# Optimization experiments

Measured on AMD Instinct MI355X. Metric: run time of the kernel, lower is better.

## Reference

```python
import jax, jax.numpy as jnp
import numpy as np

N = 50000      # total atoms in batched graph
E = 800000     # edges
IN = 128       # in_feats
OUT = 64       # out_feats (per GAT head)
H = 4          # num_heads
NEG_SLOPE = 0.2
BN_EPS = 1e-5


def setup_inputs() -> dict:
    key = jax.random.key(0)
    ks = jax.random.split(key, 16)
    s = 0.1  # keep activations well-scaled
    return {
        "node_feats": jax.random.normal(ks[0], (N, IN), jnp.float32),
        "W_fc":       jax.random.normal(ks[1], (IN, H * OUT), jnp.float32) * s,
        "attn_l":     jax.random.normal(ks[2], (H, OUT), jnp.float32) * s,
        "attn_r":     jax.random.normal(ks[3], (H, OUT), jnp.float32) * s,
        "gat_res_w":  jax.random.normal(ks[4], (IN, H * OUT), jnp.float32) * s,
        "gat_bias":   jax.random.normal(ks[5], (H * OUT,), jnp.float32) * s,
        "conv_w":     jax.random.normal(ks[6], (1, H, 1), jnp.float32) * s,
        "conv_b":     jax.random.normal(ks[7], (1,), jnp.float32) * s,
        "res_w":      jax.random.normal(ks[8], (IN, OUT), jnp.float32) * s,
        "res_b":      jax.random.normal(ks[9], (OUT,), jnp.float32) * s,
        "bn_gamma":   jnp.ones((OUT,), jnp.float32),
        "bn_beta":    jnp.zeros((OUT,), jnp.float32),
        "src":        jax.random.randint(ks[10], (E,), 0, N, jnp.int32),
        "dst":        jax.random.randint(ks[11], (E,), 0, N, jnp.int32),
        "etype":      0,
    }


def reference(node_feats, W_fc, attn_l, attn_r, gat_res_w, gat_bias,
              conv_w, conv_b, res_w, res_b, bn_gamma, bn_beta,
              src, dst, etype):
    # ---- GATConv (DGL semantics, eval mode: no dropout) ----
    h = (node_feats @ W_fc).reshape(-1, H, OUT)            # [N,H,D]
    el = jnp.sum(h * attn_l, axis=-1)                      # [N,H]
    er = jnp.sum(h * attn_r, axis=-1)                      # [N,H]
    e = jax.nn.leaky_relu(el[src] + er[dst], NEG_SLOPE)    # [E,H]
    # segment softmax over incoming edges of each dst node
    m = jax.ops.segment_max(e, dst, num_segments=N)        # [N,H]
    m = jnp.where(jnp.isfinite(m), m, 0.0)                 # empty segments
    a = jnp.exp(e - m[dst])                                # [E,H]
    ssum = jax.ops.segment_sum(a, dst, num_segments=N)     # [N,H]
    alpha = a / (ssum[dst] + 1e-16)                        # [E,H]
    # weighted aggregation: rst[v] = sum_{(u->v)} alpha * h[u]
    rst = jax.ops.segment_sum(alpha[:, :, None] * h[src], dst, num_segments=N)  # [N,H,D]
    # GAT residual (in != H*OUT -> linear res_fc, no bias) + bias + activation
    rst = rst + (node_feats @ gat_res_w).reshape(-1, H, OUT) + gat_bias.reshape(H, OUT)
    rst = jax.nn.relu(rst)                                 # [N,H,D]
    # ---- Conv1d(4 -> 1, kernel=1): weighted head merge ----
    y = jnp.einsum("nhd,h->nd", rst, conv_w[0, :, 0]) + conv_b[0]  # [N,D]
    # ---- outer residual ----
    y = y + jax.nn.relu(node_feats @ res_w + res_b)
    # ---- BatchNorm1d (training-style batch stats) ----
    mean = jnp.mean(y, axis=0)
    var = jnp.var(y, axis=0)
    return (y - mean) / jnp.sqrt(var + BN_EPS) * bn_gamma + bn_beta
```

## Files before the change

### kernel.cpp

```cpp
#include <hip/hip_runtime.h>

#define IN_F   128
#define OUTD   64
#define HOUT   256
#define NEG_SLOPE 0.2f
#define BN_EPS 1e-5f
#define HB     1024
#define SB     512

typedef __attribute__((ext_vector_type(8))) short bf16x8;
typedef __attribute__((ext_vector_type(4))) float f32x4;
typedef __attribute__((ext_vector_type(2))) float f32x2;

__device__ __forceinline__ unsigned short f2bf(float f) {
    union { float f; unsigned u; } v; v.f = f;
    unsigned r = (v.u + 0x7FFF + ((v.u >> 16) & 1)) >> 16;
    return (unsigned short)r;
}
__device__ __forceinline__ float bf2f(unsigned short h) {
    union { unsigned u; float f; } v; v.u = ((unsigned)h) << 16;
    return v.f;
}
__device__ __forceinline__ float u2f(unsigned u) {
    union { unsigned u; float f; } v; v.u = u;
    return v.f;
}
__device__ __forceinline__ unsigned f2u(float f) {
    union { float f; unsigned u; } v; v.f = f;
    return v.u;
}

__device__ __forceinline__ int b2idx(int c, int k) {
    int tt, j;
    if (c < 256)      { tt = (c >> 4) & 3;                     j = c >> 6; }
    else if (c < 512) { int cc = c - 256; tt = 4 + ((cc >> 4) & 3); j = cc >> 6; }
    else if (c < 576) { int cc = c - 512; tt = 8;              j = cc >> 4; }
    else              { tt = 9;                                j = 0; }
    int n15 = c & 15;
    int ks = k >> 5, qd = (k >> 3) & 3, kk = k & 7;
    return ((((tt * 4 + j) * 4 + ks) * 64) + qd * 16 + n15) * 8 + kk;
}

__global__ __launch_bounds__(256) void k0_pack(
    const float* __restrict__ W_fc, const float* __restrict__ W_gres,
    const float* __restrict__ W_res,
    const float* __restrict__ attn_l, const float* __restrict__ attn_r,
    unsigned short* __restrict__ Btg2,
    const int* __restrict__ dst, int* __restrict__ degree,
    int* __restrict__ rank, int E)
{
    int bid = blockIdx.x, t = threadIdx.x;
    if (bid < 288) {
        int idx = bid * 256 + t;
        int c = idx >> 7, k = idx & 127;
        float v;
        if (c < 256)      v = W_fc[k * HOUT + c];
        else if (c < 512) v = W_gres[k * HOUT + (c - 256)];
        else              v = W_res[k * OUTD + (c - 512)];
        Btg2[b2idx(c, k)] = f2bf(v);
        return;
    }
    if (bid == 288) {
        for (int p = t; p < 512; p += 256) {
            int h = p >> 7, k = p & 127;
            float sl = 0.f, sr = 0.f;
            for (int d = 0; d < 64; ++d) {
                float wv = W_fc[k * HOUT + h * 64 + d];
                sl += wv * attn_l[h * 64 + d];
                sr += wv * attn_r[h * 64 + d];
            }
            Btg2[b2idx(576 + h, k)] = f2bf(sl);
            Btg2[b2idx(580 + h, k)] = f2bf(sr);
        }
        for (int p = t; p < 8 * 128; p += 256) {
            int c = 584 + (p >> 7), k = p & 127;
            Btg2[b2idx(c, k)] = 0;
        }
        return;
    }
    int ht = (bid - 289) * 256 + t;
    for (int e = ht; e < E; e += HB * 256)
        rank[e] = atomicAdd(degree + dst[e], 1);
}

__global__ __launch_bounds__(256) void k1_gemm(
    const float* __restrict__ A, const unsigned short* __restrict__ Btg2,
    const float* __restrict__ gat_bias, const float* __restrict__ res_b,
    const int* __restrict__ src, const int* __restrict__ dst,
    const int* __restrict__ rank, const int* __restrict__ excl,
    const int* __restrict__ blocksum, int* __restrict__ base,
    unsigned* __restrict__ usrc_sorted,
    unsigned char* __restrict__ Hh8, unsigned char* __restrict__ Hr8,
    unsigned short* __restrict__ Rres,
    float* __restrict__ el, float* __restrict__ er,
    int N, int E, int Gblocks, int nb)
{
    int t = threadIdx.x;

    if (blockIdx.x >= Gblocks) {
        __shared__ int sm[256];
        __shared__ int base_lds[256];
        int sb = blockIdx.x - Gblocks;
        int d0 = (t < nb) ? blocksum[t] : 0;
        sm[t] = d0; __syncthreads();
        for (int off = 1; off < 256; off <<= 1) {
            int v = (t >= off) ? sm[t - off] : 0;
            __syncthreads();
            sm[t] += v;
            __syncthreads();
        }
        base_lds[t] = sm[t] - d0;
        if (sb == 0) base[t] = sm[t] - d0;
        __syncthreads();
        for (int e = sb * 256 + t; e < E; e += SB * 256) {
            int d = dst[e];
            int p = excl[d] + base_lds[d >> 8] + rank[e];
            usrc_sorted[p] = (unsigned)src[e] << 8;
        }
        return;
    }

    int w = t >> 6, lane = t & 63, quad = lane >> 4, n15 = lane & 15;
    int gw = blockIdx.x * 4 + w;
    int T = (N + 15) / 16;
    if (gw >= T) return;

    int m0 = gw * 16;
    bool full = (m0 + 16 <= N);
    int lofs = (quad * 16 + n15) * 8;

    bf16x8 af[4];
    {
        int r = m0 + n15;
#pragma unroll
        for (int ks = 0; ks < 4; ++ks) {
            float4 v0 = make_float4(0.f, 0.f, 0.f, 0.f), v1 = v0;
            if (r < N) {
                const float* ap = A + (size_t)r * IN_F + ks * 32 + quad * 8;
                v0 = *(const float4*)ap;
                v1 = *(const float4*)(ap + 4);
            }
            bf16x8 o;
            o[0] = f2bf(v0.x); o[1] = f2bf(v0.y); o[2] = f2bf(v0.z); o[3] = f2bf(v0.w);
            o[4] = f2bf(v1.x); o[5] = f2bf(v1.y); o[6] = f2bf(v1.z); o[7] = f2bf(v1.w);
            af[ks] = o;
        }
    }

#pragma unroll
    for (int s = 0; s < 4; ++s) {
        bf16x8 bfr[4][4];
#pragma unroll
        for (int ks = 0; ks < 4; ++ks)
#pragma unroll
            for (int j = 0; j < 4; ++j)
                bfr[ks][j] = *(const bf16x8*)(Btg2 + ((s * 16 + j * 4 + ks) << 9) + lofs);
        f32x4 acc[4] = {};
#pragma unroll
        for (int ks = 0; ks < 4; ++ks)
#pragma unroll
            for (int j = 0; j < 4; ++j)
                acc[j] = __builtin_amdgcn_mfma_f32_16x16x32_bf16(af[ks], bfr[ks][j], acc[j], 0, 0, 0);
#pragma unroll
        for (int reg = 0; reg < 4; ++reg) {
            int r = m0 + quad * 4 + reg;
            if (full || r < N) {
                unsigned pk = (unsigned)__builtin_amdgcn_cvt_pk_fp8_f32(acc[0][reg], acc[1][reg], 0, false);
                pk = (unsigned)__builtin_amdgcn_cvt_pk_fp8_f32(acc[2][reg], acc[3][reg], (int)pk, true);
                *(unsigned*)(Hh8 + ((size_t)r << 8) + (s * 16 + n15) * 4) = pk;
            }
        }
    }

#pragma unroll
    for (int s = 0; s < 4; ++s) {
        bf16x8 bfr[4][4];
#pragma unroll
        for (int ks = 0; ks < 4; ++ks)
#pragma unroll
            for (int j = 0; j < 4; ++j)
                bfr[ks][j] = *(const bf16x8*)(Btg2 + (((4 + s) * 16 + j * 4 + ks) << 9) + lofs);
        f32x4 acc[4] = {};
#pragma unroll
        for (int ks = 0; ks < 4; ++ks)
#pragma unroll
            for (int j = 0; j < 4; ++j)
                acc[j] = __builtin_amdgcn_mfma_f32_16x16x32_bf16(af[ks], bfr[ks][j], acc[j], 0, 0, 0);
        float b0 = gat_bias[0 * 64 + s * 16 + n15];
        float b1 = gat_bias[1 * 64 + s * 16 + n15];
        float b2 = gat_bias[2 * 64 + s * 16 + n15];
        float b3 = gat_bias[3 * 64 + s * 16 + n15];
#pragma unroll
        for (int reg = 0; reg < 4; ++reg) {
            int r = m0 + quad * 4 + reg;
            if (full || r < N) {
                unsigned pk = (unsigned)__builtin_amdgcn_cvt_pk_fp8_f32(acc[0][reg] + b0, acc[1][reg] + b1, 0, false);
                pk = (unsigned)__builtin_amdgcn_cvt_pk_fp8_f32(acc[2][reg] + b2, acc[3][reg] + b3, (int)pk, true);
                *(unsigned*)(Hr8 + ((size_t)r << 8) + (s * 16 + n15) * 4) = pk;
            }
        }
    }

    {
        bf16x8 bfr[4][4];
#pragma unroll
        for (int ks = 0; ks < 4; ++ks)
#pragma unroll
            for (int j = 0; j < 4; ++j)
                bfr[ks][j] = *(const bf16x8*)(Btg2 + ((8 * 16 + j * 4 + ks) << 9) + lofs);
        f32x4 acc[4] = {};
#pragma unroll
        for (int ks = 0; ks < 4; ++ks)
#pragma unroll
            for (int j = 0; j < 4; ++j)
                acc[j] = __builtin_amdgcn_mfma_f32_16x16x32_bf16(af[ks], bfr[ks][j], acc[j], 0, 0, 0);
#pragma unroll
        for (int reg = 0; reg < 4; ++reg) {
            int r = m0 + quad * 4 + reg;
            if (full || r < N) {
#pragma unroll
                for (int j = 0; j < 4; ++j)
                    Rres[(size_t)r * OUTD + j * 16 + n15] = f2bf(acc[j][reg] + res_b[j * 16 + n15]);
            }
        }
    }

    {
        bf16x8 b4[4];
#pragma unroll
        for (int ks = 0; ks < 4; ++ks)
            b4[ks] = *(const bf16x8*)(Btg2 + ((9 * 16 + ks) << 9) + lofs);
        f32x4 acc2 = {};
#pragma unroll
        for (int ks = 0; ks < 4; ++ks)
            acc2 = __builtin_amdgcn_mfma_f32_16x16x32_bf16(af[ks], b4[ks], acc2, 0, 0, 0);
#pragma unroll
        for (int reg = 0; reg < 4; ++reg) {
            int r = m0 + quad * 4 + reg;
            if ((full || r < N) && n15 < 8) {
                float v = acc2[reg];
                if (n15 < 4) el[(size_t)r * 4 + n15] = v;
                else         er[(size_t)r * 4 + (n15 - 4)] = v;
            }
        }
    }
}

__global__ __launch_bounds__(256) void scanA_kernel(const int* __restrict__ degree,
                                                    int* __restrict__ excl,
                                                    int* __restrict__ blocksum, int N) {
    __shared__ int sm[256];
    int t = threadIdx.x;
    int i = blockIdx.x * 256 + t;
    int d = (i < N) ? degree[i] : 0;
    sm[t] = d; __syncthreads();
    for (int off = 1; off < 256; off <<= 1) {
        int v = (t >= off) ? sm[t - off] : 0;
        __syncthreads();
        sm[t] += v;
        __syncthreads();
    }
    if (i < N) excl[i] = sm[t] - d;
    if (t == 255) blocksum[blockIdx.x] = sm[255];
}

__global__ __launch_bounds__(256) void agg_kernel(
    const unsigned char* __restrict__ Hh8, const unsigned char* __restrict__ Hr8,
    const unsigned short* __restrict__ Rres, const float* __restrict__ el,
    const float* __restrict__ er,
    const int* __restrict__ excl, const int* __restrict__ base,
    const unsigned* __restrict__ usrc_sorted,
    const float* __restrict__ conv_w, const float* __restrict__ conv_b,
    float* __restrict__ y, float* __restrict__ bnsum8, float* __restrict__ bnsq8,
    int N, int E)
{
    __shared__ float smem[256];
    __shared__ float smem2[256];
    int t = threadIdx.x;
    int wave = t >> 6, lane = t & 63;
    int v = blockIdx.x * 4 + wave;

    float yv = 0.f;
    if (v < N) {
        int b  = excl[v] + base[v >> 8];
        int e2 = (v + 1 < N) ? (excl[v + 1] + base[(v + 1) >> 8]) : E;
        int deg = e2 - b;

        float4 rv = *(const float4*)(er + (size_t)v * 4);
        const unsigned char* hbase = Hh8 + lane * 4;
        float a0 = 0.f, a1 = 0.f, a2 = 0.f, a3 = 0.f;
        float p0 = 0.f, p1 = 0.f, p2 = 0.f, p3 = 0.f;

        for (int i0 = 0; i0 < deg; i0 += 64) {
            int j = i0 + lane;
            unsigned ux = 0;
            float s0 = 0.f, s1 = 0.f, s2 = 0.f, s3 = 0.f;
            if (j < deg) {
                ux = usrc_sorted[b + j];
                float4 l = *(const float4*)(el + ((size_t)(ux >> 8)) * 4);
                float x;
                x = l.x + rv.x; x = x > 0.f ? x : NEG_SLOPE * x; s0 = __expf(x);
                x = l.y + rv.y; x = x > 0.f ? x : NEG_SLOPE * x; s1 = __expf(x);
                x = l.z + rv.z; x = x > 0.f ? x : NEG_SLOPE * x; s2 = __expf(x);
                x = l.w + rv.w; x = x > 0.f ? x : NEG_SLOPE * x; s3 = __expf(x);
                p0 += s0; p1 += s1; p2 += s2; p3 += s3;
            }
            int cl = deg - i0; if (cl > 64) cl = 64;
            int jj = 0;
            for (; jj + 3 < cl; jj += 4) {
                unsigned u_[4], hv[4];
                float w0[4], w1[4], w2[4], w3[4];
#pragma unroll
                for (int k = 0; k < 4; ++k) {
                    u_[k] = (unsigned)__builtin_amdgcn_readlane((int)ux, jj + k);
                    w0[k] = u2f((unsigned)__builtin_amdgcn_readlane((int)f2u(s0), jj + k));
                    w1[k] = u2f((unsigned)__builtin_amdgcn_readlane((int)f2u(s1), jj + k));
                    w2[k] = u2f((unsigned)__builtin_amdgcn_readlane((int)f2u(s2), jj + k));
                    w3[k] = u2f((unsigned)__builtin_amdgcn_readlane((int)f2u(s3), jj + k));
                }
#pragma unroll
                for (int k = 0; k < 4; ++k)
                    hv[k] = *(const unsigned*)(hbase + u_[k]);
#pragma unroll
                for (int k = 0; k < 4; ++k) {
                    f32x2 lo = __builtin_amdgcn_cvt_pk_f32_fp8(hv[k], false);
                    f32x2 hi = __builtin_amdgcn_cvt_pk_f32_fp8(hv[k], true);
                    a0 += w0[k] * lo.x;
                    a1 += w1[k] * lo.y;
                    a2 += w2[k] * hi.x;
                    a3 += w3[k] * hi.y;
                }
            }
            for (; jj < cl; ++jj) {
                unsigned uA = (unsigned)__builtin_amdgcn_readlane((int)ux, jj);
                float w0 = u2f((unsigned)__builtin_amdgcn_readlane((int)f2u(s0), jj));
                float w1 = u2f((unsigned)__builtin_amdgcn_readlane((int)f2u(s1), jj));
                float w2 = u2f((unsigned)__builtin_amdgcn_readlane((int)f2u(s2), jj));
                float w3 = u2f((unsigned)__builtin_amdgcn_readlane((int)f2u(s3), jj));
                unsigned hvA = *(const unsigned*)(hbase + uA);
                f32x2 lo = __builtin_amdgcn_cvt_pk_f32_fp8(hvA, false);
                f32x2 hi = __builtin_amdgcn_cvt_pk_f32_fp8(hvA, true);
                a0 += w0 * lo.x;
                a1 += w1 * lo.y;
                a2 += w2 * hi.x;
                a3 += w3 * hi.y;
            }
        }
#pragma unroll
        for (int off = 1; off < 64; off <<= 1) {
            p0 += __shfl_xor(p0, off); p1 += __shfl_xor(p1, off);
            p2 += __shfl_xor(p2, off); p3 += __shfl_xor(p3, off);
        }
        float r0 = 1.f / (p0 + 1e-16f), r1 = 1.f / (p1 + 1e-16f);
        float r2 = 1.f / (p2 + 1e-16f), r3 = 1.f / (p3 + 1e-16f);

        unsigned hr = *(const unsigned*)(Hr8 + ((size_t)v << 8) + lane * 4);
        f32x2 rlo = __builtin_amdgcn_cvt_pk_f32_fp8(hr, false);
        f32x2 rhi = __builtin_amdgcn_cvt_pk_f32_fp8(hr, true);
        float resv = bf2f(Rres[(size_t)v * OUTD + lane]);
        yv = conv_b[0] + (resv > 0.f ? resv : 0.f);
        float tt;
        tt = a0 * r0 + rlo.x; tt = tt > 0.f ? tt : 0.f; yv += conv_w[0] * tt;
        tt = a1 * r1 + rlo.y; tt = tt > 0.f ? tt : 0.f; yv += conv_w[1] * tt;
        tt = a2 * r2 + rhi.x; tt = tt > 0.f ? tt : 0.f; yv += conv_w[2] * tt;
        tt = a3 * r3 + rhi.y; tt = tt > 0.f ? tt : 0.f; yv += conv_w[3] * tt;
        y[(size_t)v * OUTD + lane] = yv;
    }

    smem[t] = yv;
    smem2[t] = yv * yv;
    __syncthreads();
    if (t < 64) {
        float s = smem[t] + smem[t + 64] + smem[t + 128] + smem[t + 192];
        float q = smem2[t] + smem2[t + 64] + smem2[t + 128] + smem2[t + 192];
        int c = (blockIdx.x & 7) << 6;
        atomicAdd(bnsum8 + c + t, s);
        atomicAdd(bnsq8 + c + t, q);
    }
}

__global__ __launch_bounds__(256) void norm_kernel(
    const float* __restrict__ y,
    const float* __restrict__ bnsum8, const float* __restrict__ bnsq8,
    const float* __restrict__ gamma, const float* __restrict__ beta,
    float* __restrict__ out, int total4, float invN) {
    __shared__ float scale[64], shift[64];
    int t = threadIdx.x;
    if (t < 64) {
        float s = 0.f, q = 0.f;
#pragma unroll
        for (int c = 0; c < 8; ++c) { s += bnsum8[c * 64 + t]; q += bnsq8[c * 64 + t]; }
        float mean = s * invN;
        float var = q * invN - mean * mean;
        float sc = gamma[t] * rsqrtf(var + BN_EPS);
        scale[t] = sc;
        shift[t] = beta[t] - mean * sc;
    }
    __syncthreads();
    int idx = blockIdx.x * blockDim.x + t;
    if (idx >= total4) return;
    float4 v = *(const float4*)(y + (size_t)idx * 4);
    int d = (idx * 4) & 63;
    float4 o;
    o.x = v.x * scale[d + 0] + shift[d + 0];
    o.y = v.y * scale[d + 1] + shift[d + 1];
    o.z = v.z * scale[d + 2] + shift[d + 2];
    o.w = v.w * scale[d + 3] + shift[d + 3];
    *(float4*)(out + (size_t)idx * 4) = o;
}

extern "C" void kernel_launch(void* const* d_in, const int* in_sizes, int n_in,
                              void* d_out, int out_size, void* d_ws, size_t ws_size,
                              hipStream_t stream) {
    const float* node_feats = (const float*)d_in[0];
    const float* W_fc       = (const float*)d_in[1];
    const float* attn_l     = (const float*)d_in[2];
    const float* attn_r     = (const float*)d_in[3];
    const float* gat_res_w  = (const float*)d_in[4];
    const float* gat_bias   = (const float*)d_in[5];
    const float* conv_w     = (const float*)d_in[6];
    const float* conv_b     = (const float*)d_in[7];
    const float* res_w      = (const float*)d_in[8];
    const float* res_b      = (const float*)d_in[9];
    const float* bn_gamma   = (const float*)d_in[10];
    const float* bn_beta    = (const float*)d_in[11];
    const int*   src        = (const int*)d_in[12];
    const int*   dst        = (const int*)d_in[13];

    const int N = in_sizes[0] / IN_F;
    const int E = in_sizes[12];
    const int nb = (N + 255) / 256;
    const int T = (N + 15) / 16;
    const int Gblocks = (T + 3) / 4;

    char* ws = (char*)d_ws;
    size_t off = 0;
    auto alloc = [&](size_t bytes) -> void* {
        void* p = (void*)(ws + off);
        off += (bytes + 255) & ~(size_t)255;
        return p;
    };

    int*   degree  = (int*)alloc((size_t)N * 4);
    float* bnsum8  = (float*)alloc(8 * 64 * 4);
    float* bnsq8   = (float*)alloc(8 * 64 * 4);
    size_t zero_bytes = off;
    int*            rank        = (int*)alloc((size_t)E * 4);
    int*            excl        = (int*)alloc((size_t)N * 4);
    int*            blocksum    = (int*)alloc(256 * 4);
    int*            base        = (int*)alloc(256 * 4);
    unsigned*       usrc_sorted = (unsigned*)alloc((size_t)E * 4);
    unsigned short* Btg2        = (unsigned short*)alloc((size_t)10 * 16 * 512 * 2);
    unsigned char*  Hh8         = (unsigned char*)alloc((size_t)N * 256);
    unsigned char*  Hr8         = (unsigned char*)alloc((size_t)N * 256);
    unsigned short* Rres        = (unsigned short*)alloc((size_t)N * OUTD * 2);
    float*          el          = (float*)alloc((size_t)N * 4 * 4);
    float*          er          = (float*)alloc((size_t)N * 4 * 4);
    float*          y           = (float*)alloc((size_t)N * OUTD * 4);
    (void)ws_size; (void)n_in; (void)out_size;

    hipMemsetAsync(d_ws, 0, zero_bytes, stream);

    k0_pack<<<289 + HB, 256, 0, stream>>>(W_fc, gat_res_w, res_w, attn_l, attn_r, Btg2,
                                          dst, degree, rank, E);
    scanA_kernel<<<nb, 256, 0, stream>>>(degree, excl, blocksum, N);
    k1_gemm<<<Gblocks + SB, 256, 0, stream>>>(node_feats, Btg2, gat_bias, res_b,
                                              src, dst, rank, excl, blocksum, base,
                                              usrc_sorted, Hh8, Hr8, Rres,
                                              el, er, N, E, Gblocks, nb);
    agg_kernel<<<(N + 3) / 4, 256, 0, stream>>>(Hh8, Hr8, Rres, el, er, excl, base,
                                                usrc_sorted, conv_w, conv_b, y,
                                                bnsum8, bnsq8, N, E);
    norm_kernel<<<(N * OUTD / 4 + 255) / 256, 256, 0, stream>>>(y, bnsum8, bnsq8,
                                                                bn_gamma, bn_beta, (float*)d_out,
                                                                N * OUTD / 4, 1.f / (float)N);
}
```

Before: 226.9 us.

## Process four destination nodes per wave in GAT aggregation kernel

Each wave now handles four consecutive destination nodes instead of one, walking their combined edge range in 64-edge chunks. The low two bits of each sorted source entry carry the local node index, and four accumulator vectors are selected per edge. Per-node softmax denominators are gathered with LDS atomics rather than wave shuffles. This targets underused lanes and per-chunk overhead for low-degree nodes (average degree is about 16), at the cost of a per-edge switch, LDS atomic contention and a scattered er load per edge.

```diff
diff --git a/kernel.cpp b/kernel.cpp
--- a/kernel.cpp
+++ b/kernel.cpp
@@ -115,7 +115,7 @@
         for (int e = sb * 256 + t; e < E; e += SB * 256) {
             int d = dst[e];
             int p = excl[d] + base_lds[d >> 8] + rank[e];
-            usrc_sorted[p] = (unsigned)src[e] << 8;
+            usrc_sorted[p] = ((unsigned)src[e] << 8) | (unsigned)(d & 3);
         }
         return;
     }
@@ -274,22 +274,23 @@
     float* __restrict__ y, float* __restrict__ bnsum8, float* __restrict__ bnsq8,
     int N, int E)
 {
+    __shared__ float p_lds[4][4][4];
     __shared__ float smem[256];
     __shared__ float smem2[256];
     int t = threadIdx.x;
     int wave = t >> 6, lane = t & 63;
-    int v = blockIdx.x * 4 + wave;
-
-    float yv = 0.f;
-    if (v < N) {
-        int b  = excl[v] + base[v >> 8];
-        int e2 = (v + 1 < N) ? (excl[v + 1] + base[(v + 1) >> 8]) : E;
+    int v0 = (blockIdx.x * 4 + wave) * 4;
+
+    if (lane < 16) p_lds[wave][lane >> 2][lane & 3] = 0.f;
+
+    float bn_s = 0.f, bn_q = 0.f;
+    if (v0 < N) {
+        int b = excl[v0] + base[v0 >> 8];
+        int e2 = (v0 + 4 < N) ? (excl[v0 + 4] + base[(v0 + 4) >> 8]) : E;
         int deg = e2 - b;
 
-        float4 rv = *(const float4*)(er + (size_t)v * 4);
-        const unsigned char* hbase = Hh8 + lane * 4;
-        float a0 = 0.f, a1 = 0.f, a2 = 0.f, a3 = 0.f;
-        float p0 = 0.f, p1 = 0.f, p2 = 0.f, p3 = 0.f;
+        unsigned loff = (unsigned)(lane << 2);
+        f32x4 a0 = {}, a1 = {}, a2 = {}, a3 = {};
 
         for (int i0 = 0; i0 < deg; i0 += 64) {
             int j = i0 + lane;
@@ -297,78 +298,92 @@
             float s0 = 0.f, s1 = 0.f, s2 = 0.f, s3 = 0.f;
             if (j < deg) {
                 ux = usrc_sorted[b + j];
+                int nid = (int)(ux & 3u);
                 float4 l = *(const float4*)(el + ((size_t)(ux >> 8)) * 4);
+                float4 rv = *(const float4*)(er + (size_t)(v0 + nid) * 4);
                 float x;
                 x = l.x + rv.x; x = x > 0.f ? x : NEG_SLOPE * x; s0 = __expf(x);
                 x = l.y + rv.y; x = x > 0.f ? x : NEG_SLOPE * x; s1 = __expf(x);
                 x = l.z + rv.z; x = x > 0.f ? x : NEG_SLOPE * x; s2 = __expf(x);
                 x = l.w + rv.w; x = x > 0.f ? x : NEG_SLOPE * x; s3 = __expf(x);
-                p0 += s0; p1 += s1; p2 += s2; p3 += s3;
+                atomicAdd(&p_lds[wave][nid][0], s0);
+                atomicAdd(&p_lds[wave][nid][1], s1);
+                atomicAdd(&p_lds[wave][nid][2], s2);
+                atomicAdd(&p_lds[wave][nid][3], s3);
             }
             int cl = deg - i0; if (cl > 64) cl = 64;
+
+#define CONSUME(UK, GK, IDX)                                                          \
+            {                                                                         \
+                float w0 = u2f((unsigned)__builtin_amdgcn_readlane((int)f2u(s0), (IDX))); \
+                float w1 = u2f((unsigned)__builtin_amdgcn_readlane((int)f2u(s1), (IDX))); \
+                float w2 = u2f((unsigned)__builtin_amdgcn_readlane((int)f2u(s2), (IDX))); \
+                float w3 = u2f((unsigned)__builtin_amdgcn_readlane((int)f2u(s3), (IDX))); \
+                f32x2 lo = __builtin_amdgcn_cvt_pk_f32_fp8((GK), false);              \
+                f32x2 hi = __builtin_amdgcn_cvt_pk_f32_fp8((GK), true);               \
+                switch ((UK) & 3u) {                                                  \
+                case 0: a0[0] += w0 * lo.x; a0[1] += w1 * lo.y; a0[2] += w2 * hi.x; a0[3] += w3 * hi.y; break; \
+                case 1: a1[0] += w0 * lo.x; a1[1] += w1 * lo.y; a1[2] += w2 * hi.x; a1[3] += w3 * hi.y; break; \
+                case 2: a2[0] += w0 * lo.x; a2[1] += w1 * lo.y; a2[2] += w2 * hi.x; a2[3] += w3 * hi.y; break; \
+                default: a3[0] += w0 * lo.x; a3[1] += w1 * lo.y; a3[2] += w2 * hi.x; a3[3] += w3 * hi.y; break; \
+                }                                                                     \
+            }
+
             int jj = 0;
             for (; jj + 3 < cl; jj += 4) {
-                unsigned u_[4], hv[4];
-                float w0[4], w1[4], w2[4], w3[4];
-#pragma unroll
-                for (int k = 0; k < 4; ++k) {
-                    u_[k] = (unsigned)__builtin_amdgcn_readlane((int)ux, jj + k);
-                    w0[k] = u2f((unsigned)__builtin_amdgcn_readlane((int)f2u(s0), jj + k));
-                    w1[k] = u2f((unsigned)__builtin_amdgcn_readlane((int)f2u(s1), jj + k));
-                    w2[k] = u2f((unsigned)__builtin_amdgcn_readlane((int)f2u(s2), jj + k));
-                    w3[k] = u2f((unsigned)__builtin_amdgcn_readlane((int)f2u(s3), jj + k));
-                }
-#pragma unroll
-                for (int k = 0; k < 4; ++k)
-                    hv[k] = *(const unsigned*)(hbase + u_[k]);
-#pragma unroll
-                for (int k = 0; k < 4; ++k) {
-                    f32x2 lo = __builtin_amdgcn_cvt_pk_f32_fp8(hv[k], false);
-                    f32x2 hi = __builtin_amdgcn_cvt_pk_f32_fp8(hv[k], true);
-                    a0 += w0[k] * lo.x;
-                    a1 += w1[k] * lo.y;
-                    a2 += w2[k] * hi.x;
-                    a3 += w3[k] * hi.y;
-                }
+                unsigned uk0 = (unsigned)__builtin_amdgcn_readlane((int)ux, jj + 0);
+                unsigned uk1 = (unsigned)__builtin_amdgcn_readlane((int)ux, jj + 1);
+                unsigned uk2 = (unsigned)__builtin_amdgcn_readlane((int)ux, jj + 2);
+                unsigned uk3 = (unsigned)__builtin_amdgcn_readlane((int)ux, jj + 3);
+                unsigned g0 = *(const unsigned*)(Hh8 + (size_t)(uk0 & ~255u) + loff);
+                unsigned g1 = *(const unsigned*)(Hh8 + (size_t)(uk1 & ~255u) + loff);
+                unsigned g2 = *(const unsigned*)(Hh8 + (size_t)(uk2 & ~255u) + loff);
+                unsigned g3 = *(const unsigned*)(Hh8 + (size_t)(uk3 & ~255u) + loff);
+                CONSUME(uk0, g0, jj + 0)
+                CONSUME(uk1, g1, jj + 1)
+                CONSUME(uk2, g2, jj + 2)
+                CONSUME(uk3, g3, jj + 3)
             }
             for (; jj < cl; ++jj) {
-                unsigned uA = (unsigned)__builtin_amdgcn_readlane((int)ux, jj);
-                float w0 = u2f((unsigned)__builtin_amdgcn_readlane((int)f2u(s0), jj));
-                float w1 = u2f((unsigned)__builtin_amdgcn_readlane((int)f2u(s1), jj));
-                float w2 = u2f((unsigned)__builtin_amdgcn_readlane((int)f2u(s2), jj));
-                float w3 = u2f((unsigned)__builtin_amdgcn_readlane((int)f2u(s3), jj));
-                unsigned hvA = *(const unsigned*)(hbase + uA);
-                f32x2 lo = __builtin_amdgcn_cvt_pk_f32_fp8(hvA, false);
-                f32x2 hi = __builtin_amdgcn_cvt_pk_f32_fp8(hvA, true);
-                a0 += w0 * lo.x;
-                a1 += w1 * lo.y;
-                a2 += w2 * hi.x;
-                a3 += w3 * hi.y;
-            }
-        }
-#pragma unroll
-        for (int off = 1; off < 64; off <<= 1) {
-            p0 += __shfl_xor(p0, off); p1 += __shfl_xor(p1, off);
-            p2 += __shfl_xor(p2, off); p3 += __shfl_xor(p3, off);
-        }
-        float r0 = 1.f / (p0 + 1e-16f), r1 = 1.f / (p1 + 1e-16f);
-        float r2 = 1.f / (p2 + 1e-16f), r3 = 1.f / (p3 + 1e-16f);
-
-        unsigned hr = *(const unsigned*)(Hr8 + ((size_t)v << 8) + lane * 4);
-        f32x2 rlo = __builtin_amdgcn_cvt_pk_f32_fp8(hr, false);
-        f32x2 rhi = __builtin_amdgcn_cvt_pk_f32_fp8(hr, true);
-        float resv = bf2f(Rres[(size_t)v * OUTD + lane]);
-        yv = conv_b[0] + (resv > 0.f ? resv : 0.f);
-        float tt;
-        tt = a0 * r0 + rlo.x; tt = tt > 0.f ? tt : 0.f; yv += conv_w[0] * tt;
-        tt = a1 * r1 + rlo.y; tt = tt > 0.f ? tt : 0.f; yv += conv_w[1] * tt;
-        tt = a2 * r2 + rhi.x; tt = tt > 0.f ? tt : 0.f; yv += conv_w[2] * tt;
-        tt = a3 * r3 + rhi.y; tt = tt > 0.f ? tt : 0.f; yv += conv_w[3] * tt;
-        y[(size_t)v * OUTD + lane] = yv;
-    }
-
-    smem[t] = yv;
-    smem2[t] = yv * yv;
+                unsigned uk = (unsigned)__builtin_amdgcn_readlane((int)ux, jj);
+                unsigned g = *(const unsigned*)(Hh8 + (size_t)(uk & ~255u) + loff);
+                CONSUME(uk, g, jj)
+            }
+#undef CONSUME
+        }
+
+        float cb = conv_b[0];
+        float cw0 = conv_w[0], cw1 = conv_w[1], cw2 = conv_w[2], cw3 = conv_w[3];
+#define EPI(I, ACC)                                                                   \
+        {                                                                             \
+            int vv = v0 + (I);                                                        \
+            if (vv < N) {                                                             \
+                float4 pp = *(const float4*)&p_lds[wave][(I)][0];                     \
+                float r0 = 1.f / (pp.x + 1e-16f), r1 = 1.f / (pp.y + 1e-16f);         \
+                float r2 = 1.f / (pp.z + 1e-16f), r3 = 1.f / (pp.w + 1e-16f);         \
+                unsigned hr = *(const unsigned*)(Hr8 + ((size_t)vv << 8) + loff);     \
+                f32x2 rlo = __builtin_amdgcn_cvt_pk_f32_fp8(hr, false);               \
+                f32x2 rhi = __builtin_amdgcn_cvt_pk_f32_fp8(hr, true);                \
+                float resv = bf2f(Rres[(size_t)vv * OUTD + lane]);                    \
+                float yv = cb + (resv > 0.f ? resv : 0.f);                            \
+                float tt;                                                             \
+                tt = ACC[0] * r0 + rlo.x; tt = tt > 0.f ? tt : 0.f; yv += cw0 * tt;   \
+                tt = ACC[1] * r1 + rlo.y; tt = tt > 0.f ? tt : 0.f; yv += cw1 * tt;   \
+                tt = ACC[2] * r2 + rhi.x; tt = tt > 0.f ? tt : 0.f; yv += cw2 * tt;   \
+                tt = ACC[3] * r3 + rhi.y; tt = tt > 0.f ? tt : 0.f; yv += cw3 * tt;   \
+                y[(size_t)vv * OUTD + lane] = yv;                                     \
+                bn_s += yv; bn_q += yv * yv;                                          \
+            }                                                                         \
+        }
+        EPI(0, a0)
+        EPI(1, a1)
+        EPI(2, a2)
+        EPI(3, a3)
+#undef EPI
+    }
+
+    smem[t] = bn_s;
+    smem2[t] = bn_q;
     __syncthreads();
     if (t < 64) {
         float s = smem[t] + smem[t + 64] + smem[t + 128] + smem[t + 192];
@@ -468,9 +483,9 @@
                                               src, dst, rank, excl, blocksum, base,
                                               usrc_sorted, Hh8, Hr8, Rres,
                                               el, er, N, E, Gblocks, nb);
-    agg_kernel<<<(N + 3) / 4, 256, 0, stream>>>(Hh8, Hr8, Rres, el, er, excl, base,
-                                                usrc_sorted, conv_w, conv_b, y,
-                                                bnsum8, bnsq8, N, E);
+    agg_kernel<<<(N + 15) / 16, 256, 0, stream>>>(Hh8, Hr8, Rres, el, er, excl, base,
+                                                  usrc_sorted, conv_w, conv_b, y,
+                                                  bnsum8, bnsq8, N, E);
     norm_kernel<<<(N * OUTD / 4 + 255) / 256, 256, 0, stream>>>(y, bnsum8, bnsq8,
                                                                 bn_gamma, bn_beta, (float*)d_out,
                                                                 N * OUTD / 4, 1.f / (float)N);
```

Result: no change. 230.7 us (+1.7%).

## Move degree histogram into GEMM kernel and split scatter into its own kernel

Applied to the files above, without the earlier changes.

Moves the atomic degree/rank histogram from the weight-packing kernel into extra blocks of the GEMM kernel, so the histogram overlaps with the GEMM instead of with the tiny pack. The CSR scatter becomes a separate one-edge-per-thread kernel launched after the scan, instead of running alongside the GEMM. This reshuffles which work overlaps across the pipeline stages. It adds one kernel launch, and every scatter block now repeats the 256-entry blocksum prefix scan.

```diff
diff --git a/kernel.cpp b/kernel.cpp
--- a/kernel.cpp
+++ b/kernel.cpp
@@ -5,8 +5,7 @@
 #define HOUT   256
 #define NEG_SLOPE 0.2f
 #define BN_EPS 1e-5f
-#define HB     1024
-#define SB     512
+#define HISTB  256
 
 typedef __attribute__((ext_vector_type(8))) short bf16x8;
 typedef __attribute__((ext_vector_type(4))) float f32x4;
@@ -45,9 +44,7 @@
     const float* __restrict__ W_fc, const float* __restrict__ W_gres,
     const float* __restrict__ W_res,
     const float* __restrict__ attn_l, const float* __restrict__ attn_r,
-    unsigned short* __restrict__ Btg2,
-    const int* __restrict__ dst, int* __restrict__ degree,
-    int* __restrict__ rank, int E)
+    unsigned short* __restrict__ Btg2)
 {
     int bid = blockIdx.x, t = threadIdx.x;
     if (bid < 288) {
@@ -60,63 +57,38 @@
         Btg2[b2idx(c, k)] = f2bf(v);
         return;
     }
-    if (bid == 288) {
-        for (int p = t; p < 512; p += 256) {
-            int h = p >> 7, k = p & 127;
-            float sl = 0.f, sr = 0.f;
-            for (int d = 0; d < 64; ++d) {
-                float wv = W_fc[k * HOUT + h * 64 + d];
-                sl += wv * attn_l[h * 64 + d];
-                sr += wv * attn_r[h * 64 + d];
-            }
-            Btg2[b2idx(576 + h, k)] = f2bf(sl);
-            Btg2[b2idx(580 + h, k)] = f2bf(sr);
-        }
-        for (int p = t; p < 8 * 128; p += 256) {
-            int c = 584 + (p >> 7), k = p & 127;
-            Btg2[b2idx(c, k)] = 0;
-        }
-        return;
-    }
-    int ht = (bid - 289) * 256 + t;
-    for (int e = ht; e < E; e += HB * 256)
-        rank[e] = atomicAdd(degree + dst[e], 1);
+    for (int p = t; p < 512; p += 256) {
+        int h = p >> 7, k = p & 127;
+        float sl = 0.f, sr = 0.f;
+        for (int d = 0; d < 64; ++d) {
+            float wv = W_fc[k * HOUT + h * 64 + d];
+            sl += wv * attn_l[h * 64 + d];
+            sr += wv * attn_r[h * 64 + d];
+        }
+        Btg2[b2idx(576 + h, k)] = f2bf(sl);
+        Btg2[b2idx(580 + h, k)] = f2bf(sr);
+    }
+    for (int p = t; p < 8 * 128; p += 256) {
+        int c = 584 + (p >> 7), k = p & 127;
+        Btg2[b2idx(c, k)] = 0;
+    }
 }
 
 __global__ __launch_bounds__(256) void k1_gemm(
     const float* __restrict__ A, const unsigned short* __restrict__ Btg2,
     const float* __restrict__ gat_bias, const float* __restrict__ res_b,
-    const int* __restrict__ src, const int* __restrict__ dst,
-    const int* __restrict__ rank, const int* __restrict__ excl,
-    const int* __restrict__ blocksum, int* __restrict__ base,
-    unsigned* __restrict__ usrc_sorted,
+    const int* __restrict__ dst, int* __restrict__ degree, int* __restrict__ rank,
     unsigned char* __restrict__ Hh8, unsigned char* __restrict__ Hr8,
     unsigned short* __restrict__ Rres,
     float* __restrict__ el, float* __restrict__ er,
-    int N, int E, int Gblocks, int nb)
+    int N, int E, int Gblocks)
 {
     int t = threadIdx.x;
 
     if (blockIdx.x >= Gblocks) {
-        __shared__ int sm[256];
-        __shared__ int base_lds[256];
-        int sb = blockIdx.x - Gblocks;
-        int d0 = (t < nb) ? blocksum[t] : 0;
-        sm[t] = d0; __syncthreads();
-        for (int off = 1; off < 256; off <<= 1) {
-            int v = (t >= off) ? sm[t - off] : 0;
-            __syncthreads();
-            sm[t] += v;
-            __syncthreads();
-        }
-        base_lds[t] = sm[t] - d0;
-        if (sb == 0) base[t] = sm[t] - d0;
-        __syncthreads();
-        for (int e = sb * 256 + t; e < E; e += SB * 256) {
-            int d = dst[e];
-            int p = excl[d] + base_lds[d >> 8] + rank[e];
-            usrc_sorted[p] = (unsigned)src[e] << 8;
-        }
+        int ht = (blockIdx.x - Gblocks) * 256 + t;
+        for (int e = ht; e < E; e += HISTB * 256)
+            rank[e] = atomicAdd(degree + dst[e], 1);
         return;
     }
 
@@ -262,6 +234,33 @@
     }
     if (i < N) excl[i] = sm[t] - d;
     if (t == 255) blocksum[blockIdx.x] = sm[255];
+}
+
+__global__ __launch_bounds__(256) void scatter_kernel(
+    const int* __restrict__ src, const int* __restrict__ dst,
+    const int* __restrict__ rank, const int* __restrict__ excl,
+    const int* __restrict__ blocksum, int* __restrict__ base,
+    unsigned* __restrict__ usrc_sorted, int E, int nb) {
+    __shared__ int sm[256];
+    __shared__ int base_lds[256];
+    int t = threadIdx.x;
+    int d0 = (t < nb) ? blocksum[t] : 0;
+    sm[t] = d0; __syncthreads();
+    for (int off = 1; off < 256; off <<= 1) {
+        int v = (t >= off) ? sm[t - off] : 0;
+        __syncthreads();
+        sm[t] += v;
+        __syncthreads();
+    }
+    base_lds[t] = sm[t] - d0;
+    if (blockIdx.x == 0) base[t] = sm[t] - d0;
+    __syncthreads();
+
+    int e = blockIdx.x * 256 + t;
+    if (e >= E) return;
+    int d = dst[e];
+    int p = excl[d] + base_lds[d >> 8] + rank[e];
+    usrc_sorted[p] = (unsigned)src[e] << 8;
 }
 
 __global__ __launch_bounds__(256) void agg_kernel(
@@ -461,13 +460,13 @@
 
     hipMemsetAsync(d_ws, 0, zero_bytes, stream);
 
-    k0_pack<<<289 + HB, 256, 0, stream>>>(W_fc, gat_res_w, res_w, attn_l, attn_r, Btg2,
-                                          dst, degree, rank, E);
+    k0_pack<<<289, 256, 0, stream>>>(W_fc, gat_res_w, res_w, attn_l, attn_r, Btg2);
+    k1_gemm<<<Gblocks + HISTB, 256, 0, stream>>>(node_feats, Btg2, gat_bias, res_b,
+                                                 dst, degree, rank, Hh8, Hr8, Rres,
+                                                 el, er, N, E, Gblocks);
     scanA_kernel<<<nb, 256, 0, stream>>>(degree, excl, blocksum, N);
-    k1_gemm<<<Gblocks + SB, 256, 0, stream>>>(node_feats, Btg2, gat_bias, res_b,
-                                              src, dst, rank, excl, blocksum, base,
-                                              usrc_sorted, Hh8, Hr8, Rres,
-                                              el, er, N, E, Gblocks, nb);
+    scatter_kernel<<<(E + 255) / 256, 256, 0, stream>>>(src, dst, rank, excl, blocksum,
+                                                        base, usrc_sorted, E, nb);
     agg_kernel<<<(N + 3) / 4, 256, 0, stream>>>(Hh8, Hr8, Rres, el, er, excl, base,
                                                 usrc_sorted, conv_w, conv_b, y,
                                                 bnsum8, bnsq8, N, E);
```

Result: no change. 224.6 us (-1.0%).
